# Kernel tuning notes

Hardware: AMD Instinct MI355X
Metric: run time of the kernel (lower is better)

## Reference

```python
import jax, jax.numpy as jnp
import numpy as np

HIDDEN = 1024
NUM_HEADS = 16
HEAD_SIZE = HIDDEN // NUM_HEADS
B, S = 2, 2048


def setup_inputs() -> dict:
    key = jax.random.key(0)
    k_x, k_wqkv, k_bqkv, k_wo, k_bo = jax.random.split(key, 5)
    x = jax.random.normal(k_x, (B, S, HIDDEN), dtype=jnp.float32)
    # Dense kernels, fan-in scaled like lecun_normal init
    Wqkv = jax.random.normal(k_wqkv, (HIDDEN, 3 * HIDDEN), dtype=jnp.float32) / np.sqrt(HIDDEN)
    bqkv = jnp.zeros((3 * HIDDEN,), dtype=jnp.float32)
    Wo = jax.random.normal(k_wo, (HIDDEN, HIDDEN), dtype=jnp.float32) / np.sqrt(HIDDEN)
    bo = jnp.zeros((HIDDEN,), dtype=jnp.float32)
    return {"x": x, "Wqkv": Wqkv, "bqkv": bqkv, "Wo": Wo, "bo": bo}


def reference(x, Wqkv, bqkv, Wo, bo):
    b, s, h = x.shape
    qkv = jnp.einsum('bsh,hf->bsf', x, Wqkv) + bqkv          # [b, s, 3*h]
    qkv = qkv.reshape(b, s, 3, NUM_HEADS, HEAD_SIZE)
    q, k, v = qkv[:, :, 0], qkv[:, :, 1], qkv[:, :, 2]        # [b, s, nh, hd]
    scale = 1.0 / np.sqrt(HEAD_SIZE)
    scores = jnp.einsum('bqhd,bkhd->bhqk', q, k) * scale      # [b, nh, s, s]
    weights = jax.nn.softmax(scores, axis=-1)
    attn = jnp.einsum('bhqk,bkhd->bqhd', weights, v)          # [b, s, nh, hd]
    attn = attn.reshape(b, s, h)
    return jnp.einsum('bsh,hf->bsf', attn, Wo) + bo
```

## Files before the change

### kernel.cpp

```cpp
#include <hip/hip_runtime.h>
#include <hip/hip_bf16.h>

#define HIDDEN 1024
#define NH 16
#define BATCH 2
#define SEQ 2048

typedef __attribute__((ext_vector_type(8))) short bf16x8;
typedef __attribute__((ext_vector_type(4))) float f32x4;

__device__ __forceinline__ ushort f2bf(float f) {
    __hip_bfloat16 h = __float2bfloat16(f);
    return *reinterpret_cast<ushort*>(&h);
}
__device__ __forceinline__ float fexp2(float x) {
#if __has_builtin(__builtin_amdgcn_exp2f)
    return __builtin_amdgcn_exp2f(x);
#else
    return exp2f(x);
#endif
}
__device__ __forceinline__ uint pack_bf_trunc(float a, float b) {
    return __builtin_amdgcn_perm(__float_as_uint(b), __float_as_uint(a), 0x07060302u);
}

__device__ __forceinline__ void async_copy16(const ushort* g, ushort* l) {
    __builtin_amdgcn_global_load_lds((const __attribute__((address_space(1))) void*)g,
                                     (__attribute__((address_space(3))) void*)l,
                                     16, 0, 0);
}

__global__ void prep_kernel(const float* __restrict__ x,
                            const float* __restrict__ Wqkv,
                            const float* __restrict__ Wo,
                            ushort* __restrict__ xb,
                            ushort* __restrict__ Wt,
                            ushort* __restrict__ WoT)
{
    __shared__ float t[32][33];
    const int bid = blockIdx.x;
    const int tid = threadIdx.x;

    if (bid < 4096) {
        int i = (bid * 256 + tid) * 4;
        float4 v = *(const float4*)(x + i);
        ushort4 w;
        w.x = f2bf(v.x); w.y = f2bf(v.y); w.z = f2bf(v.z); w.w = f2bf(v.w);
        *(ushort4*)(xb + i) = w;
        return;
    }
    const int r = tid >> 3;
    const int c = (tid & 7) * 4;
    if (bid < 7168) {
        int tt = bid - 4096;
        int k0 = (tt & 31) * 32;
        int n0 = (tt >> 5) * 32;
        const int N = 3 * HIDDEN, K = HIDDEN;
        float4 v = *(const float4*)(Wqkv + (size_t)(k0 + r) * N + n0 + c);
        t[r][c] = v.x; t[r][c + 1] = v.y; t[r][c + 2] = v.z; t[r][c + 3] = v.w;
        __syncthreads();
        ushort4 w;
        w.x = f2bf(t[c + 0][r]); w.y = f2bf(t[c + 1][r]);
        w.z = f2bf(t[c + 2][r]); w.w = f2bf(t[c + 3][r]);
        *(ushort4*)(Wt + (size_t)(n0 + r) * K + k0 + c) = w;
    } else {
        int tt = bid - 7168;
        int k0 = (tt & 31) * 32;
        int n0 = (tt >> 5) * 32;
        const int N = HIDDEN, K = HIDDEN;
        float4 v = *(const float4*)(Wo + (size_t)(k0 + r) * N + n0 + c);
        t[r][c] = v.x; t[r][c + 1] = v.y; t[r][c + 2] = v.z; t[r][c + 3] = v.w;
        __syncthreads();
        ushort4 w;
        w.x = f2bf(t[c + 0][r]); w.y = f2bf(t[c + 1][r]);
        w.z = f2bf(t[c + 2][r]); w.w = f2bf(t[c + 3][r]);
        *(ushort4*)(WoT + (size_t)(n0 + r) * K + k0 + c) = w;
    }
}

__global__ __launch_bounds__(256, 3)
void gemm_mfma_bf16_kernel(const ushort* __restrict__ A,
                           const ushort* __restrict__ Bt,
                           const float* __restrict__ bias,
                           ushort* __restrict__ C, int N,
                           int qscale_cols, float qscale,
                           ushort* __restrict__ vtg, int vt_mode)
{
    constexpr int K = 1024;
    __shared__ ushort As[128 * 64];
    __shared__ ushort Bs[128 * 64];

    const int tid  = threadIdx.x;
    const int wave = tid >> 6;
    const int lane = tid & 63;
    const int l16  = lane & 15;
    const int quad = lane >> 4;
    const int wm = wave & 1, wn = wave >> 1;

    const int bm = blockIdx.y * 128;
    const int bn = blockIdx.x * 128;

    const int srow = lane >> 3;
    const int lblk = (lane & 7) ^ srow;
    const ushort* Ag = A  + (size_t)(bm + wave * 32 + srow) * K + lblk * 8;
    const ushort* Bg = Bt + (size_t)(bn + wave * 32 + srow) * K + lblk * 8;
    ushort* Asl = As + wave * 32 * 64;
    ushort* Bsl = Bs + wave * 32 * 64;

    f32x4 acc[4][4];
    #pragma unroll
    for (int i = 0; i < 4; i++)
        #pragma unroll
        for (int j = 0; j < 4; j++) acc[i][j] = (f32x4){0.f, 0.f, 0.f, 0.f};

    for (int k0 = 0; k0 < K; k0 += 64) {
        __syncthreads();
        #pragma unroll
        for (int t = 0; t < 4; t++) {
            async_copy16(Ag + (size_t)t * 8 * K + k0, Asl + t * 8 * 64);
            async_copy16(Bg + (size_t)t * 8 * K + k0, Bsl + t * 8 * 64);
        }
        __syncthreads();

        #pragma unroll
        for (int s = 0; s < 2; s++) {
            bf16x8 af[4], bfr[4];
            #pragma unroll
            for (int i = 0; i < 4; i++) {
                int m = wm * 64 + i * 16 + l16;
                int n = wn * 64 + i * 16 + l16;
                af[i]  = *(const bf16x8*)&As[m * 64 + (((s * 4 + quad) ^ (m & 7)) << 3)];
                bfr[i] = *(const bf16x8*)&Bs[n * 64 + (((s * 4 + quad) ^ (n & 7)) << 3)];
            }
            #pragma unroll
            for (int i = 0; i < 4; i++)
                #pragma unroll
                for (int j = 0; j < 4; j++)
                    acc[i][j] = __builtin_amdgcn_mfma_f32_16x16x32_bf16(af[i], bfr[j], acc[i][j], 0, 0, 0);
        }
    }

    #pragma unroll
    for (int j = 0; j < 4; j++) {
        int col = bn + wn * 64 + j * 16 + l16;
        float bv = bias[col];
        if (vt_mode && col >= 2048) {
            int dfull = col - 2048;
            int hh = dfull >> 6, dd = dfull & 63;
            int bb = bm >> 11;
            int sb = ((bm & 2047) + wm * 64) >> 6;
            ushort tmp[16];
            #pragma unroll
            for (int i = 0; i < 4; i++)
                #pragma unroll
                for (int r = 0; r < 4; r++)
                    tmp[r * 4 + i] = f2bf(acc[i][j][r] + bv);
            ushort* dst = vtg + ((size_t)((bb * NH + hh) * 64 + dd)) * SEQ
                          + sb * 64 + quad * 16;
            *(uint4*)dst = *(const uint4*)tmp;
            *(uint4*)(dst + 8) = *(const uint4*)(tmp + 8);
        } else {
            float s = (col < qscale_cols) ? qscale : 1.0f;
            #pragma unroll
            for (int i = 0; i < 4; i++) {
                int row0 = bm + wm * 64 + i * 16 + quad * 4;
                #pragma unroll
                for (int r = 0; r < 4; r++)
                    C[(size_t)(row0 + r) * N + col] = f2bf((acc[i][j][r] + bv) * s);
            }
        }
    }
}

__global__ __launch_bounds__(256, 4)
void gemm_out_kernel(const ushort* __restrict__ A,
                     const ushort* __restrict__ Bt,
                     const float* __restrict__ bias,
                     float* __restrict__ C)
{
    constexpr int K = 1024, N = 1024;
    __shared__ ushort As[128 * 64];
    __shared__ ushort Bs[64 * 64];

    const int tid  = threadIdx.x;
    const int wave = tid >> 6;
    const int lane = tid & 63;
    const int l16  = lane & 15;
    const int quad = lane >> 4;
    const int wm = wave & 1, wn = wave >> 1;

    const int bm = blockIdx.y * 128;
    const int bn = blockIdx.x * 64;

    const int srow = lane >> 3;
    const int lblk = (lane & 7) ^ srow;
    const ushort* Ag = A  + (size_t)(bm + wave * 32 + srow) * K + lblk * 8;
    const ushort* Bg = Bt + (size_t)(bn + wave * 16 + srow) * K + lblk * 8;
    ushort* Asl = As + wave * 32 * 64;
    ushort* Bsl = Bs + wave * 16 * 64;

    f32x4 acc[4][2];
    #pragma unroll
    for (int i = 0; i < 4; i++)
        #pragma unroll
        for (int j = 0; j < 2; j++) acc[i][j] = (f32x4){0.f, 0.f, 0.f, 0.f};

    for (int k0 = 0; k0 < K; k0 += 64) {
        __syncthreads();
        #pragma unroll
        for (int t = 0; t < 4; t++)
            async_copy16(Ag + (size_t)t * 8 * K + k0, Asl + t * 8 * 64);
        #pragma unroll
        for (int t = 0; t < 2; t++)
            async_copy16(Bg + (size_t)t * 8 * K + k0, Bsl + t * 8 * 64);
        __syncthreads();

        #pragma unroll
        for (int s = 0; s < 2; s++) {
            bf16x8 af[4], bfr[2];
            #pragma unroll
            for (int i = 0; i < 4; i++) {
                int m = wm * 64 + i * 16 + l16;
                af[i] = *(const bf16x8*)&As[m * 64 + (((s * 4 + quad) ^ (m & 7)) << 3)];
            }
            #pragma unroll
            for (int j = 0; j < 2; j++) {
                int n = wn * 32 + j * 16 + l16;
                bfr[j] = *(const bf16x8*)&Bs[n * 64 + (((s * 4 + quad) ^ (n & 7)) << 3)];
            }
            #pragma unroll
            for (int i = 0; i < 4; i++)
                #pragma unroll
                for (int j = 0; j < 2; j++)
                    acc[i][j] = __builtin_amdgcn_mfma_f32_16x16x32_bf16(af[i], bfr[j], acc[i][j], 0, 0, 0);
        }
    }

    #pragma unroll
    for (int j = 0; j < 2; j++) {
        int col = bn + wn * 32 + j * 16 + l16;
        float bv = bias[col];
        #pragma unroll
        for (int i = 0; i < 4; i++) {
            int row0 = bm + wm * 64 + i * 16 + quad * 4;
            #pragma unroll
            for (int r = 0; r < 4; r++)
                C[(size_t)(row0 + r) * N + col] = acc[i][j][r] + bv;
        }
    }
}

__global__ __launch_bounds__(256, 2)
void attn_mfma_v8_kernel(const ushort* __restrict__ qkvb,
                         const ushort* __restrict__ vtg,
                         ushort* __restrict__ attn)
{
    __shared__ __align__(16) ushort smem[34816];

    const int tid  = threadIdx.x;
    const int wave = tid >> 6;
    const int qg   = wave & 1;
    const int kh   = wave >> 1;
    const int lane = tid & 63;
    const int l16  = lane & 15;
    const int quad = lane >> 4;

    const int obid = blockIdx.x;
    const int qb = (obid >> 3) & 15;
    const int bh = (obid & 7) * 4 + (obid >> 7);
    const int h  = bh & (NH - 1);
    const int b  = bh >> 4;

    const int qbase = qb * 128 + qg * 64;
    const int hoff  = h * 64;

    ushort* KsH = smem + kh * 4096;
    ushort* VsH = smem + 8192 + kh * 4096;
    ushort* Psw = smem + 16384 + wave * 4608;

    bf16x8 a_q[4][2];
    #pragma unroll
    for (int mg = 0; mg < 4; mg++) {
        int qrow = b * SEQ + qbase + mg * 16 + l16;
        const ushort* qp = qkvb + (size_t)qrow * 3072 + hoff + quad * 8;
        a_q[mg][0] = *(const bf16x8*)qp;
        a_q[mg][1] = *(const bf16x8*)(qp + 32);
    }

    f32x4 o[4][4];
    f32x4 lacc[4];
    #pragma unroll
    for (int mg = 0; mg < 4; mg++) {
        lacc[mg] = (f32x4){0.f, 0.f, 0.f, 0.f};
        #pragma unroll
        for (int nt = 0; nt < 4; nt++) o[mg][nt] = (f32x4){0.f, 0.f, 0.f, 0.f};
    }

    bf16x8 b_ones;
    #pragma unroll
    for (int j = 0; j < 8; j++) b_ones[j] = (short)0x3f80;

    const ushort* kvb    = qkvb + (size_t)b * SEQ * 3072;
    const ushort* vtg_bh = vtg + (size_t)((b * NH + h) * 64) * SEQ;

    const int srow8 = lane >> 3;
    const int gblk  = ((lane & 7) ^ srow8) << 3;
    const ushort* kg = kvb + (size_t)(kh * 1024 + qg * 32 + srow8) * 3072 + 1024 + hoff + gblk;
    const ushort* vg = vtg_bh + (size_t)(qg * 32 + srow8) * SEQ + kh * 1024 + gblk;

    for (int t = 0; t < 16; t++) {
        const int k0 = t * 64;
        __syncthreads();
        #pragma unroll
        for (int c = 0; c < 4; c++) {
            async_copy16(kg + (size_t)(k0 + c * 8) * 3072, KsH + (qg * 32 + c * 8) * 64);
            async_copy16(vg + (size_t)(c * 8) * SEQ + k0,  VsH + (qg * 32 + c * 8) * 64);
        }
        __syncthreads();

        f32x4 sc[4][4];
        #pragma unroll
        for (int nt = 0; nt < 4; nt++) {
            int key = nt * 16 + l16;
            bf16x8 bk0 = *(const bf16x8*)&KsH[key * 64 + ((quad ^ (key & 7)) << 3)];
            bf16x8 bk1 = *(const bf16x8*)&KsH[key * 64 + (((4 + quad) ^ (key & 7)) << 3)];
            #pragma unroll
            for (int mg = 0; mg < 4; mg++) {
                f32x4 a = (f32x4){0.f, 0.f, 0.f, 0.f};
                a = __builtin_amdgcn_mfma_f32_16x16x32_bf16(a_q[mg][0], bk0, a, 0, 0, 0);
                a = __builtin_amdgcn_mfma_f32_16x16x32_bf16(a_q[mg][1], bk1, a, 0, 0, 0);
                sc[mg][nt] = a;
            }
        }

        #pragma unroll
        for (int mg = 0; mg < 4; mg++) {
            #pragma unroll
            for (int r = 0; r < 4; r++) {
                int q = mg * 16 + quad * 4 + r;
                uint2 pk2;
                pk2.x = pack_bf_trunc(fexp2(sc[mg][0][r]), fexp2(sc[mg][1][r]));
                pk2.y = pack_bf_trunc(fexp2(sc[mg][2][r]), fexp2(sc[mg][3][r]));
                *(uint2*)&Psw[q * 72 + l16 * 4] = pk2;
            }
        }

        asm volatile("s_waitcnt lgkmcnt(0)" ::: "memory");

        #pragma unroll
        for (int mg = 0; mg < 4; mg++) {
            bf16x8 ap0 = *(const bf16x8*)&Psw[(mg * 16 + l16) * 72 + quad * 8];
            bf16x8 ap1 = *(const bf16x8*)&Psw[(mg * 16 + l16) * 72 + 32 + quad * 8];
            #pragma unroll
            for (int nt = 0; nt < 4; nt++) {
                int d = nt * 16 + l16;
                bf16x8 bv0 = *(const bf16x8*)&VsH[d * 64 + ((quad ^ (d & 7)) << 3)];
                bf16x8 bv1 = *(const bf16x8*)&VsH[d * 64 + (((4 + quad) ^ (d & 7)) << 3)];
                o[mg][nt] = __builtin_amdgcn_mfma_f32_16x16x32_bf16(ap0, bv0, o[mg][nt], 0, 0, 0);
                o[mg][nt] = __builtin_amdgcn_mfma_f32_16x16x32_bf16(ap1, bv1, o[mg][nt], 0, 0, 0);
            }
            lacc[mg] = __builtin_amdgcn_mfma_f32_16x16x32_bf16(ap0, b_ones, lacc[mg], 0, 0, 0);
            lacc[mg] = __builtin_amdgcn_mfma_f32_16x16x32_bf16(ap1, b_ones, lacc[mg], 0, 0, 0);
        }
    }

    __syncthreads();
    float* osc = (float*)smem;
    float* lsc = (float*)(smem + 16384);
    const int ob = qg * 4096;
    const int lb = qg * 64;
    if (kh == 1) {
        #pragma unroll
        for (int mg = 0; mg < 4; mg++) {
            #pragma unroll
            for (int nt = 0; nt < 4; nt++)
                *(f32x4*)&osc[ob + ((mg * 4 + nt) * 4 + quad) * 64 + l16 * 4] = o[mg][nt];
            if (l16 == 0) *(f32x4*)&lsc[lb + (mg * 4 + quad) * 4] = lacc[mg];
        }
    }
    __syncthreads();
    if (kh == 0) {
        #pragma unroll
        for (int mg = 0; mg < 4; mg++) {
            #pragma unroll
            for (int nt = 0; nt < 4; nt++)
                o[mg][nt] += *(const f32x4*)&osc[ob + ((mg * 4 + nt) * 4 + quad) * 64 + l16 * 4];
            lacc[mg] += *(const f32x4*)&lsc[lb + (mg * 4 + quad) * 4];
        }
        #pragma unroll
        for (int mg = 0; mg < 4; mg++) {
            #pragma unroll
            for (int r = 0; r < 4; r++) {
                float inv = 1.f / lacc[mg][r];
                int row = b * SEQ + qbase + mg * 16 + quad * 4 + r;
                size_t base = (size_t)row * HIDDEN + hoff + l16;
                #pragma unroll
                for (int nt = 0; nt < 4; nt++)
                    attn[base + nt * 16] = f2bf(o[mg][nt][r] * inv);
            }
        }
    }
}

__global__ __launch_bounds__(512, 4)
void attn_mfma_fb_kernel(const ushort* __restrict__ qkvb,
                         ushort* __restrict__ attn)
{
    __shared__ __align__(16) ushort smem[34816];

    const int tid   = threadIdx.x;
    const int wave  = tid >> 6;
    const int wavel = wave & 3;
    const int kh    = wave >> 2;
    const int lane  = tid & 63;
    const int l16   = lane & 15;
    const int quad  = lane >> 4;

    const int qb = blockIdx.x & 15;
    const int bh = blockIdx.x >> 4;
    const int h  = bh & (NH - 1);
    const int b  = bh >> 4;

    const int qbase = qb * 128;
    const int hoff  = h * 64;

    ushort* KsH = smem + kh * 4096;
    ushort* VsH = smem + 8192 + kh * 4096;
    ushort* Psw = smem + 16384 + wave * 2304;

    bf16x8 a_q[2][2];
    #pragma unroll
    for (int mg = 0; mg < 2; mg++) {
        int qrow = b * SEQ + qbase + wavel * 32 + mg * 16 + l16;
        const ushort* qp = qkvb + (size_t)qrow * 3072 + hoff + quad * 8;
        a_q[mg][0] = *(const bf16x8*)qp;
        a_q[mg][1] = *(const bf16x8*)(qp + 32);
    }

    f32x4 o[2][4];
    f32x4 lacc[2];
    #pragma unroll
    for (int mg = 0; mg < 2; mg++) {
        lacc[mg] = (f32x4){0.f, 0.f, 0.f, 0.f};
        #pragma unroll
        for (int nt = 0; nt < 4; nt++) o[mg][nt] = (f32x4){0.f, 0.f, 0.f, 0.f};
    }

    bf16x8 b_ones;
    #pragma unroll
    for (int j = 0; j < 8; j++) b_ones[j] = (short)0x3f80;

    const ushort* kvb = qkvb + (size_t)b * SEQ * 3072;

    for (int t = 0; t < 16; t++) {
        const int k0 = t * 64;
        __syncthreads();
        {
            const int tl = tid & 255;
            #pragma unroll
            for (int i = 0; i < 2; i++) {
                int key = (tl >> 3) + 32 * i;
                int blk = tl & 7;
                const ushort* ksrc = kvb + (size_t)(kh * 1024 + k0 + key) * 3072 + 1024 + hoff + blk * 8;
                uint4 kv = *(const uint4*)ksrc;
                *(uint4*)&KsH[key * 64 + ((blk ^ (key & 7)) << 3)] = kv;
                uint4 vv = *(const uint4*)(ksrc + 1024);
                const ushort* vpp = (const ushort*)&vv;
                int pk_ = (key & 15) * 4 + (key >> 4);
                #pragma unroll
                for (int j = 0; j < 8; j++) {
                    int d = blk * 8 + j;
                    VsH[d * 64 + (((pk_ >> 3) ^ (d & 7)) << 3) + (pk_ & 7)] = vpp[j];
                }
            }
        }
        __syncthreads();

        f32x4 sc[2][4];
        #pragma unroll
        for (int nt = 0; nt < 4; nt++) {
            int key = nt * 16 + l16;
            bf16x8 bk0 = *(const bf16x8*)&KsH[key * 64 + ((quad ^ (key & 7)) << 3)];
            bf16x8 bk1 = *(const bf16x8*)&KsH[key * 64 + (((4 + quad) ^ (key & 7)) << 3)];
            #pragma unroll
            for (int mg = 0; mg < 2; mg++) {
                f32x4 a = (f32x4){0.f, 0.f, 0.f, 0.f};
                a = __builtin_amdgcn_mfma_f32_16x16x32_bf16(a_q[mg][0], bk0, a, 0, 0, 0);
                a = __builtin_amdgcn_mfma_f32_16x16x32_bf16(a_q[mg][1], bk1, a, 0, 0, 0);
                sc[mg][nt] = a;
            }
        }

        #pragma unroll
        for (int mg = 0; mg < 2; mg++) {
            #pragma unroll
            for (int r = 0; r < 4; r++) {
                int q = mg * 16 + quad * 4 + r;
                uint2 pk2;
                pk2.x = pack_bf_trunc(fexp2(sc[mg][0][r]), fexp2(sc[mg][1][r]));
                pk2.y = pack_bf_trunc(fexp2(sc[mg][2][r]), fexp2(sc[mg][3][r]));
                *(uint2*)&Psw[q * 72 + l16 * 4] = pk2;
            }
        }

        asm volatile("s_waitcnt lgkmcnt(0)" ::: "memory");
        bf16x8 a_p[2][2];
        #pragma unroll
        for (int mg = 0; mg < 2; mg++) {
            a_p[mg][0] = *(const bf16x8*)&Psw[(mg * 16 + l16) * 72 + quad * 8];
            a_p[mg][1] = *(const bf16x8*)&Psw[(mg * 16 + l16) * 72 + 32 + quad * 8];
        }

        #pragma unroll
        for (int nt = 0; nt < 4; nt++) {
            int d = nt * 16 + l16;
            bf16x8 bv0 = *(const bf16x8*)&VsH[d * 64 + ((quad ^ (d & 7)) << 3)];
            bf16x8 bv1 = *(const bf16x8*)&VsH[d * 64 + (((4 + quad) ^ (d & 7)) << 3)];
            #pragma unroll
            for (int mg = 0; mg < 2; mg++) {
                o[mg][nt] = __builtin_amdgcn_mfma_f32_16x16x32_bf16(a_p[mg][0], bv0, o[mg][nt], 0, 0, 0);
                o[mg][nt] = __builtin_amdgcn_mfma_f32_16x16x32_bf16(a_p[mg][1], bv1, o[mg][nt], 0, 0, 0);
            }
        }
        #pragma unroll
        for (int mg = 0; mg < 2; mg++) {
            lacc[mg] = __builtin_amdgcn_mfma_f32_16x16x32_bf16(a_p[mg][0], b_ones, lacc[mg], 0, 0, 0);
            lacc[mg] = __builtin_amdgcn_mfma_f32_16x16x32_bf16(a_p[mg][1], b_ones, lacc[mg], 0, 0, 0);
        }
    }

    __syncthreads();
    float* osc = (float*)smem;
    float* lsc = (float*)(smem + 16384);
    const int fo = wavel * 2048 + quad * 64 + l16 * 4;
    const int fl = wavel * 512 + quad * 64 + l16 * 4;
    if (kh == 1) {
        #pragma unroll
        for (int mg = 0; mg < 2; mg++) {
            #pragma unroll
            for (int nt = 0; nt < 4; nt++)
                *(f32x4*)&osc[fo + (mg * 4 + nt) * 256] = o[mg][nt];
            *(f32x4*)&lsc[fl + mg * 256] = lacc[mg];
        }
    }
    __syncthreads();
    if (kh == 0) {
        #pragma unroll
        for (int mg = 0; mg < 2; mg++) {
            #pragma unroll
            for (int nt = 0; nt < 4; nt++)
                o[mg][nt] += *(const f32x4*)&osc[fo + (mg * 4 + nt) * 256];
            lacc[mg] += *(const f32x4*)&lsc[fl + mg * 256];
        }
        #pragma unroll
        for (int mg = 0; mg < 2; mg++) {
            #pragma unroll
            for (int r = 0; r < 4; r++) {
                float inv = 1.f / lacc[mg][r];
                int row = b * SEQ + qbase + wavel * 32 + mg * 16 + quad * 4 + r;
                size_t base = (size_t)row * HIDDEN + hoff + l16;
                #pragma unroll
                for (int nt = 0; nt < 4; nt++)
                    attn[base + nt * 16] = f2bf(o[mg][nt][r] * inv);
            }
        }
    }
}

extern "C" void kernel_launch(void* const* d_in, const int* in_sizes, int n_in,
                              void* d_out, int out_size, void* d_ws, size_t ws_size,
                              hipStream_t stream) {
    const float* x    = (const float*)d_in[0];
    const float* Wqkv = (const float*)d_in[1];
    const float* bqkv = (const float*)d_in[2];
    const float* Wo   = (const float*)d_in[3];
    const float* bo   = (const float*)d_in[4];
    float* out = (float*)d_out;

    const int M = BATCH * SEQ;
    const size_t MB = 1024 * 1024;

    char* ws = (char*)d_ws;
    ushort* qkvb = (ushort*)ws;
    ushort* attn = (ushort*)(ws + 24 * MB);
    ushort* xb   = (ushort*)(ws + 24 * MB);
    ushort* Wt   = (ushort*)(ws + 32 * MB);
    ushort* WoT  = (ushort*)(ws + 38 * MB);
    ushort* vtg  = (ushort*)(ws + 40 * MB);
    const int use_vtg = (ws_size >= 48 * MB) ? 1 : 0;

    const float qscale = 0.125f * 1.44269504088896f;

    prep_kernel<<<8192, 256, 0, stream>>>(x, Wqkv, Wo, xb, Wt, WoT);

    {
        dim3 grid((3 * HIDDEN) / 128, M / 128);
        gemm_mfma_bf16_kernel<<<grid, 256, 0, stream>>>(xb, Wt, bqkv, qkvb,
                                                        3 * HIDDEN, HIDDEN, qscale,
                                                        vtg, use_vtg);
    }

    if (use_vtg) {
        attn_mfma_v8_kernel<<<BATCH * NH * (SEQ / 128), 256, 0, stream>>>(
            qkvb, vtg, attn);
    } else {
        attn_mfma_fb_kernel<<<BATCH * NH * (SEQ / 128), 512, 0, stream>>>(
            qkvb, attn);
    }

    {
        dim3 grid(HIDDEN / 64, M / 128);
        gemm_out_kernel<<<grid, 256, 0, stream>>>(attn, WoT, bo, out);
    }
}
```

Before: 181.0 us.

## Restructure attention to 8 waves with 16 queries each and double-buffered K/V

Replaces the 4-wave attention kernel, in which each wave held 64 queries and the key range was split across wave pairs, with an 8-wave kernel where each wave owns 16 queries and all waves share a full-key-range loop. K/V tiles are double-buffered in shared memory, so the next tile's async copy is issued before the current tile is computed, and the cross-wave O/l reduction at the end is removed. Registers per wave and LDS per block shrink, allowing more waves resident. In exchange each wave reuses every K/V LDS read across only 16 queries instead of 64, which raises LDS read traffic per MFMA.

```diff
diff --git a/kernel.cpp b/kernel.cpp
--- a/kernel.cpp
+++ b/kernel.cpp
@@ -250,17 +250,15 @@
     }
 }
 
-__global__ __launch_bounds__(256, 2)
-void attn_mfma_v8_kernel(const ushort* __restrict__ qkvb,
+__global__ __launch_bounds__(512, 4)
+void attn_mfma_v9_kernel(const ushort* __restrict__ qkvb,
                          const ushort* __restrict__ vtg,
                          ushort* __restrict__ attn)
 {
-    __shared__ __align__(16) ushort smem[34816];
+    __shared__ __align__(16) ushort smem[25600];
 
     const int tid  = threadIdx.x;
     const int wave = tid >> 6;
-    const int qg   = wave & 1;
-    const int kh   = wave >> 1;
     const int lane = tid & 63;
     const int l16  = lane & 15;
     const int quad = lane >> 4;
@@ -271,30 +269,23 @@
     const int h  = bh & (NH - 1);
     const int b  = bh >> 4;
 
-    const int qbase = qb * 128 + qg * 64;
+    const int qbase = qb * 128 + wave * 16;
     const int hoff  = h * 64;
 
-    ushort* KsH = smem + kh * 4096;
-    ushort* VsH = smem + 8192 + kh * 4096;
-    ushort* Psw = smem + 16384 + wave * 4608;
-
-    bf16x8 a_q[4][2];
-    #pragma unroll
-    for (int mg = 0; mg < 4; mg++) {
-        int qrow = b * SEQ + qbase + mg * 16 + l16;
+    ushort* Psw = smem + 16384 + wave * 1152;
+
+    bf16x8 a_q0, a_q1;
+    {
+        int qrow = b * SEQ + qbase + l16;
         const ushort* qp = qkvb + (size_t)qrow * 3072 + hoff + quad * 8;
-        a_q[mg][0] = *(const bf16x8*)qp;
-        a_q[mg][1] = *(const bf16x8*)(qp + 32);
-    }
-
-    f32x4 o[4][4];
-    f32x4 lacc[4];
-    #pragma unroll
-    for (int mg = 0; mg < 4; mg++) {
-        lacc[mg] = (f32x4){0.f, 0.f, 0.f, 0.f};
-        #pragma unroll
-        for (int nt = 0; nt < 4; nt++) o[mg][nt] = (f32x4){0.f, 0.f, 0.f, 0.f};
-    }
+        a_q0 = *(const bf16x8*)qp;
+        a_q1 = *(const bf16x8*)(qp + 32);
+    }
+
+    f32x4 o[4];
+    f32x4 lacc = (f32x4){0.f, 0.f, 0.f, 0.f};
+    #pragma unroll
+    for (int nt = 0; nt < 4; nt++) o[nt] = (f32x4){0.f, 0.f, 0.f, 0.f};
 
     bf16x8 b_ones;
     #pragma unroll
@@ -305,100 +296,74 @@
 
     const int srow8 = lane >> 3;
     const int gblk  = ((lane & 7) ^ srow8) << 3;
-    const ushort* kg = kvb + (size_t)(kh * 1024 + qg * 32 + srow8) * 3072 + 1024 + hoff + gblk;
-    const ushort* vg = vtg_bh + (size_t)(qg * 32 + srow8) * SEQ + kh * 1024 + gblk;
-
-    for (int t = 0; t < 16; t++) {
-        const int k0 = t * 64;
-        __syncthreads();
-        #pragma unroll
-        for (int c = 0; c < 4; c++) {
-            async_copy16(kg + (size_t)(k0 + c * 8) * 3072, KsH + (qg * 32 + c * 8) * 64);
-            async_copy16(vg + (size_t)(c * 8) * SEQ + k0,  VsH + (qg * 32 + c * 8) * 64);
-        }
-        __syncthreads();
-
-        f32x4 sc[4][4];
+    const ushort* kg = kvb + (size_t)(wave * 8 + srow8) * 3072 + 1024 + hoff + gblk;
+    const ushort* vg = vtg_bh + (size_t)(wave * 8 + srow8) * SEQ + gblk;
+
+    ushort* k_dst = smem + wave * 512;
+    ushort* v_dst = smem + 8192 + wave * 512;
+
+    async_copy16(kg, k_dst);
+    async_copy16(vg, v_dst);
+    __syncthreads();
+
+    int cur = 0;
+    for (int t = 0; t < 32; t++) {
+        if (t < 31) {
+            const int k0n = (t + 1) * 64;
+            async_copy16(kg + (size_t)k0n * 3072, k_dst + ((cur ^ 1) << 12));
+            async_copy16(vg + k0n,                v_dst + ((cur ^ 1) << 12));
+        }
+        const ushort* Ks = smem + (cur << 12);
+        const ushort* Vs = smem + 8192 + (cur << 12);
+
+        f32x4 sc[4];
         #pragma unroll
         for (int nt = 0; nt < 4; nt++) {
             int key = nt * 16 + l16;
-            bf16x8 bk0 = *(const bf16x8*)&KsH[key * 64 + ((quad ^ (key & 7)) << 3)];
-            bf16x8 bk1 = *(const bf16x8*)&KsH[key * 64 + (((4 + quad) ^ (key & 7)) << 3)];
-            #pragma unroll
-            for (int mg = 0; mg < 4; mg++) {
-                f32x4 a = (f32x4){0.f, 0.f, 0.f, 0.f};
-                a = __builtin_amdgcn_mfma_f32_16x16x32_bf16(a_q[mg][0], bk0, a, 0, 0, 0);
-                a = __builtin_amdgcn_mfma_f32_16x16x32_bf16(a_q[mg][1], bk1, a, 0, 0, 0);
-                sc[mg][nt] = a;
-            }
-        }
-
-        #pragma unroll
-        for (int mg = 0; mg < 4; mg++) {
-            #pragma unroll
-            for (int r = 0; r < 4; r++) {
-                int q = mg * 16 + quad * 4 + r;
-                uint2 pk2;
-                pk2.x = pack_bf_trunc(fexp2(sc[mg][0][r]), fexp2(sc[mg][1][r]));
-                pk2.y = pack_bf_trunc(fexp2(sc[mg][2][r]), fexp2(sc[mg][3][r]));
-                *(uint2*)&Psw[q * 72 + l16 * 4] = pk2;
-            }
+            bf16x8 bk0 = *(const bf16x8*)&Ks[key * 64 + ((quad ^ (key & 7)) << 3)];
+            bf16x8 bk1 = *(const bf16x8*)&Ks[key * 64 + (((4 + quad) ^ (key & 7)) << 3)];
+            f32x4 a = (f32x4){0.f, 0.f, 0.f, 0.f};
+            a = __builtin_amdgcn_mfma_f32_16x16x32_bf16(a_q0, bk0, a, 0, 0, 0);
+            a = __builtin_amdgcn_mfma_f32_16x16x32_bf16(a_q1, bk1, a, 0, 0, 0);
+            sc[nt] = a;
+        }
+
+        #pragma unroll
+        for (int r = 0; r < 4; r++) {
+            int q = quad * 4 + r;
+            uint2 pk2;
+            pk2.x = pack_bf_trunc(fexp2(sc[0][r]), fexp2(sc[1][r]));
+            pk2.y = pack_bf_trunc(fexp2(sc[2][r]), fexp2(sc[3][r]));
+            *(uint2*)&Psw[q * 72 + l16 * 4] = pk2;
         }
 
         asm volatile("s_waitcnt lgkmcnt(0)" ::: "memory");
 
-        #pragma unroll
-        for (int mg = 0; mg < 4; mg++) {
-            bf16x8 ap0 = *(const bf16x8*)&Psw[(mg * 16 + l16) * 72 + quad * 8];
-            bf16x8 ap1 = *(const bf16x8*)&Psw[(mg * 16 + l16) * 72 + 32 + quad * 8];
-            #pragma unroll
-            for (int nt = 0; nt < 4; nt++) {
-                int d = nt * 16 + l16;
-                bf16x8 bv0 = *(const bf16x8*)&VsH[d * 64 + ((quad ^ (d & 7)) << 3)];
-                bf16x8 bv1 = *(const bf16x8*)&VsH[d * 64 + (((4 + quad) ^ (d & 7)) << 3)];
-                o[mg][nt] = __builtin_amdgcn_mfma_f32_16x16x32_bf16(ap0, bv0, o[mg][nt], 0, 0, 0);
-                o[mg][nt] = __builtin_amdgcn_mfma_f32_16x16x32_bf16(ap1, bv1, o[mg][nt], 0, 0, 0);
-            }
-            lacc[mg] = __builtin_amdgcn_mfma_f32_16x16x32_bf16(ap0, b_ones, lacc[mg], 0, 0, 0);
-            lacc[mg] = __builtin_amdgcn_mfma_f32_16x16x32_bf16(ap1, b_ones, lacc[mg], 0, 0, 0);
-        }
-    }
-
-    __syncthreads();
-    float* osc = (float*)smem;
-    float* lsc = (float*)(smem + 16384);
-    const int ob = qg * 4096;
-    const int lb = qg * 64;
-    if (kh == 1) {
-        #pragma unroll
-        for (int mg = 0; mg < 4; mg++) {
-            #pragma unroll
-            for (int nt = 0; nt < 4; nt++)
-                *(f32x4*)&osc[ob + ((mg * 4 + nt) * 4 + quad) * 64 + l16 * 4] = o[mg][nt];
-            if (l16 == 0) *(f32x4*)&lsc[lb + (mg * 4 + quad) * 4] = lacc[mg];
-        }
-    }
-    __syncthreads();
-    if (kh == 0) {
-        #pragma unroll
-        for (int mg = 0; mg < 4; mg++) {
-            #pragma unroll
-            for (int nt = 0; nt < 4; nt++)
-                o[mg][nt] += *(const f32x4*)&osc[ob + ((mg * 4 + nt) * 4 + quad) * 64 + l16 * 4];
-            lacc[mg] += *(const f32x4*)&lsc[lb + (mg * 4 + quad) * 4];
-        }
-        #pragma unroll
-        for (int mg = 0; mg < 4; mg++) {
-            #pragma unroll
-            for (int r = 0; r < 4; r++) {
-                float inv = 1.f / lacc[mg][r];
-                int row = b * SEQ + qbase + mg * 16 + quad * 4 + r;
-                size_t base = (size_t)row * HIDDEN + hoff + l16;
-                #pragma unroll
-                for (int nt = 0; nt < 4; nt++)
-                    attn[base + nt * 16] = f2bf(o[mg][nt][r] * inv);
-            }
-        }
+        bf16x8 ap0 = *(const bf16x8*)&Psw[l16 * 72 + quad * 8];
+        bf16x8 ap1 = *(const bf16x8*)&Psw[l16 * 72 + 32 + quad * 8];
+        #pragma unroll
+        for (int nt = 0; nt < 4; nt++) {
+            int d = nt * 16 + l16;
+            bf16x8 bv0 = *(const bf16x8*)&Vs[d * 64 + ((quad ^ (d & 7)) << 3)];
+            bf16x8 bv1 = *(const bf16x8*)&Vs[d * 64 + (((4 + quad) ^ (d & 7)) << 3)];
+            o[nt] = __builtin_amdgcn_mfma_f32_16x16x32_bf16(ap0, bv0, o[nt], 0, 0, 0);
+            o[nt] = __builtin_amdgcn_mfma_f32_16x16x32_bf16(ap1, bv1, o[nt], 0, 0, 0);
+        }
+        lacc = __builtin_amdgcn_mfma_f32_16x16x32_bf16(ap0, b_ones, lacc, 0, 0, 0);
+        lacc = __builtin_amdgcn_mfma_f32_16x16x32_bf16(ap1, b_ones, lacc, 0, 0, 0);
+
+        __syncthreads();
+        cur ^= 1;
+    }
+
+    #pragma unroll
+    for (int r = 0; r < 4; r++) {
+        float inv = 1.f / lacc[r];
+        int row = b * SEQ + qbase + quad * 4 + r;
+        size_t base = (size_t)row * HIDDEN + hoff + l16;
+        #pragma unroll
+        for (int nt = 0; nt < 4; nt++)
+            attn[base + nt * 16] = f2bf(o[nt][r] * inv);
     }
 }
 
@@ -601,7 +566,7 @@
     }
 
     if (use_vtg) {
-        attn_mfma_v8_kernel<<<BATCH * NH * (SEQ / 128), 256, 0, stream>>>(
+        attn_mfma_v9_kernel<<<BATCH * NH * (SEQ / 128), 512, 0, stream>>>(
             qkvb, vtg, attn);
     } else {
         attn_mfma_fb_kernel<<<BATCH * NH * (SEQ / 128), 512, 0, stream>>>(
```

Result: no change. 178.3 us (-1.5%).

## Restructure attention kernel: per-wave query split with double-buffered K/V tiles

Applied to the files above, without the earlier changes.

The attention kernel no longer splits the key range across two wave halves, which had to be merged through shared memory at the end. Each of the four waves now owns 32 query rows and walks all 2048 keys. K/V tiles are shared by all waves and double-buffered, so the next tile's async copy is issued while the current one is computed, leaving one barrier per iteration instead of two. This drops the cross-wave reduction and overlaps loads with math, at the cost of fewer rows per wave, which reduces reuse of each K/V fragment loaded from LDS.

```diff
diff --git a/kernel.cpp b/kernel.cpp
--- a/kernel.cpp
+++ b/kernel.cpp
@@ -251,16 +251,14 @@
 }
 
 __global__ __launch_bounds__(256, 2)
-void attn_mfma_v8_kernel(const ushort* __restrict__ qkvb,
-                         const ushort* __restrict__ vtg,
-                         ushort* __restrict__ attn)
+void attn_mfma_v10_kernel(const ushort* __restrict__ qkvb,
+                          const ushort* __restrict__ vtg,
+                          ushort* __restrict__ attn)
 {
-    __shared__ __align__(16) ushort smem[34816];
+    __shared__ __align__(16) ushort smem[25600];
 
     const int tid  = threadIdx.x;
     const int wave = tid >> 6;
-    const int qg   = wave & 1;
-    const int kh   = wave >> 1;
     const int lane = tid & 63;
     const int l16  = lane & 15;
     const int quad = lane >> 4;
@@ -271,26 +269,24 @@
     const int h  = bh & (NH - 1);
     const int b  = bh >> 4;
 
-    const int qbase = qb * 128 + qg * 64;
+    const int qbase = qb * 128 + wave * 32;
     const int hoff  = h * 64;
 
-    ushort* KsH = smem + kh * 4096;
-    ushort* VsH = smem + 8192 + kh * 4096;
-    ushort* Psw = smem + 16384 + wave * 4608;
-
-    bf16x8 a_q[4][2];
-    #pragma unroll
-    for (int mg = 0; mg < 4; mg++) {
+    ushort* Psw = smem + 16384 + wave * 2304;
+
+    bf16x8 a_q[2][2];
+    #pragma unroll
+    for (int mg = 0; mg < 2; mg++) {
         int qrow = b * SEQ + qbase + mg * 16 + l16;
         const ushort* qp = qkvb + (size_t)qrow * 3072 + hoff + quad * 8;
         a_q[mg][0] = *(const bf16x8*)qp;
         a_q[mg][1] = *(const bf16x8*)(qp + 32);
     }
 
-    f32x4 o[4][4];
-    f32x4 lacc[4];
-    #pragma unroll
-    for (int mg = 0; mg < 4; mg++) {
+    f32x4 o[2][4];
+    f32x4 lacc[2];
+    #pragma unroll
+    for (int mg = 0; mg < 2; mg++) {
         lacc[mg] = (f32x4){0.f, 0.f, 0.f, 0.f};
         #pragma unroll
         for (int nt = 0; nt < 4; nt++) o[mg][nt] = (f32x4){0.f, 0.f, 0.f, 0.f};
@@ -305,27 +301,42 @@
 
     const int srow8 = lane >> 3;
     const int gblk  = ((lane & 7) ^ srow8) << 3;
-    const ushort* kg = kvb + (size_t)(kh * 1024 + qg * 32 + srow8) * 3072 + 1024 + hoff + gblk;
-    const ushort* vg = vtg_bh + (size_t)(qg * 32 + srow8) * SEQ + kh * 1024 + gblk;
-
-    for (int t = 0; t < 16; t++) {
-        const int k0 = t * 64;
-        __syncthreads();
-        #pragma unroll
-        for (int c = 0; c < 4; c++) {
-            async_copy16(kg + (size_t)(k0 + c * 8) * 3072, KsH + (qg * 32 + c * 8) * 64);
-            async_copy16(vg + (size_t)(c * 8) * SEQ + k0,  VsH + (qg * 32 + c * 8) * 64);
-        }
-        __syncthreads();
-
-        f32x4 sc[4][4];
+    const ushort* kg = kvb + (size_t)(wave * 16 + srow8) * 3072 + 1024 + hoff + gblk;
+    const ushort* vg = vtg_bh + (size_t)(wave * 16 + srow8) * SEQ + gblk;
+
+    ushort* k_dst = smem + wave * 1024;
+    ushort* v_dst = smem + 8192 + wave * 1024;
+
+    #pragma unroll
+    for (int c = 0; c < 2; c++) {
+        async_copy16(kg + (size_t)(c * 8) * 3072, k_dst + c * 512);
+        async_copy16(vg + (size_t)(c * 8) * SEQ,  v_dst + c * 512);
+    }
+    __syncthreads();
+
+    int cur = 0;
+    for (int t = 0; t < 32; t++) {
+        if (t < 31) {
+            const int k0n = (t + 1) * 64;
+            #pragma unroll
+            for (int c = 0; c < 2; c++) {
+                async_copy16(kg + (size_t)(k0n + c * 8) * 3072,
+                             k_dst + c * 512 + ((cur ^ 1) << 12));
+                async_copy16(vg + (size_t)(c * 8) * SEQ + k0n,
+                             v_dst + c * 512 + ((cur ^ 1) << 12));
+            }
+        }
+        const ushort* Ks = smem + (cur << 12);
+        const ushort* Vs = smem + 8192 + (cur << 12);
+
+        f32x4 sc[2][4];
         #pragma unroll
         for (int nt = 0; nt < 4; nt++) {
             int key = nt * 16 + l16;
-            bf16x8 bk0 = *(const bf16x8*)&KsH[key * 64 + ((quad ^ (key & 7)) << 3)];
-            bf16x8 bk1 = *(const bf16x8*)&KsH[key * 64 + (((4 + quad) ^ (key & 7)) << 3)];
-            #pragma unroll
-            for (int mg = 0; mg < 4; mg++) {
+            bf16x8 bk0 = *(const bf16x8*)&Ks[key * 64 + ((quad ^ (key & 7)) << 3)];
+            bf16x8 bk1 = *(const bf16x8*)&Ks[key * 64 + (((4 + quad) ^ (key & 7)) << 3)];
+            #pragma unroll
+            for (int mg = 0; mg < 2; mg++) {
                 f32x4 a = (f32x4){0.f, 0.f, 0.f, 0.f};
                 a = __builtin_amdgcn_mfma_f32_16x16x32_bf16(a_q[mg][0], bk0, a, 0, 0, 0);
                 a = __builtin_amdgcn_mfma_f32_16x16x32_bf16(a_q[mg][1], bk1, a, 0, 0, 0);
@@ -334,7 +345,7 @@
         }
 
         #pragma unroll
-        for (int mg = 0; mg < 4; mg++) {
+        for (int mg = 0; mg < 2; mg++) {
             #pragma unroll
             for (int r = 0; r < 4; r++) {
                 int q = mg * 16 + quad * 4 + r;
@@ -347,57 +358,43 @@
 
         asm volatile("s_waitcnt lgkmcnt(0)" ::: "memory");
 
-        #pragma unroll
-        for (int mg = 0; mg < 4; mg++) {
-            bf16x8 ap0 = *(const bf16x8*)&Psw[(mg * 16 + l16) * 72 + quad * 8];
-            bf16x8 ap1 = *(const bf16x8*)&Psw[(mg * 16 + l16) * 72 + 32 + quad * 8];
-            #pragma unroll
-            for (int nt = 0; nt < 4; nt++) {
-                int d = nt * 16 + l16;
-                bf16x8 bv0 = *(const bf16x8*)&VsH[d * 64 + ((quad ^ (d & 7)) << 3)];
-                bf16x8 bv1 = *(const bf16x8*)&VsH[d * 64 + (((4 + quad) ^ (d & 7)) << 3)];
-                o[mg][nt] = __builtin_amdgcn_mfma_f32_16x16x32_bf16(ap0, bv0, o[mg][nt], 0, 0, 0);
-                o[mg][nt] = __builtin_amdgcn_mfma_f32_16x16x32_bf16(ap1, bv1, o[mg][nt], 0, 0, 0);
-            }
-            lacc[mg] = __builtin_amdgcn_mfma_f32_16x16x32_bf16(ap0, b_ones, lacc[mg], 0, 0, 0);
-            lacc[mg] = __builtin_amdgcn_mfma_f32_16x16x32_bf16(ap1, b_ones, lacc[mg], 0, 0, 0);
-        }
-    }
-
-    __syncthreads();
-    float* osc = (float*)smem;
-    float* lsc = (float*)(smem + 16384);
-    const int ob = qg * 4096;
-    const int lb = qg * 64;
-    if (kh == 1) {
-        #pragma unroll
-        for (int mg = 0; mg < 4; mg++) {
+        bf16x8 ap[2][2];
+        #pragma unroll
+        for (int mg = 0; mg < 2; mg++) {
+            ap[mg][0] = *(const bf16x8*)&Psw[(mg * 16 + l16) * 72 + quad * 8];
+            ap[mg][1] = *(const bf16x8*)&Psw[(mg * 16 + l16) * 72 + 32 + quad * 8];
+        }
+        #pragma unroll
+        for (int nt = 0; nt < 4; nt++) {
+            int d = nt * 16 + l16;
+            bf16x8 bv0 = *(const bf16x8*)&Vs[d * 64 + ((quad ^ (d & 7)) << 3)];
+            bf16x8 bv1 = *(const bf16x8*)&Vs[d * 64 + (((4 + quad) ^ (d & 7)) << 3)];
+            #pragma unroll
+            for (int mg = 0; mg < 2; mg++) {
+                o[mg][nt] = __builtin_amdgcn_mfma_f32_16x16x32_bf16(ap[mg][0], bv0, o[mg][nt], 0, 0, 0);
+                o[mg][nt] = __builtin_amdgcn_mfma_f32_16x16x32_bf16(ap[mg][1], bv1, o[mg][nt], 0, 0, 0);
+            }
+        }
+        #pragma unroll
+        for (int mg = 0; mg < 2; mg++) {
+            lacc[mg] = __builtin_amdgcn_mfma_f32_16x16x32_bf16(ap[mg][0], b_ones, lacc[mg], 0, 0, 0);
+            lacc[mg] = __builtin_amdgcn_mfma_f32_16x16x32_bf16(ap[mg][1], b_ones, lacc[mg], 0, 0, 0);
+        }
+
+        __syncthreads();
+        cur ^= 1;
+    }
+
+    #pragma unroll
+    for (int mg = 0; mg < 2; mg++) {
+        #pragma unroll
+        for (int r = 0; r < 4; r++) {
+            float inv = 1.f / lacc[mg][r];
+            int row = b * SEQ + qbase + mg * 16 + quad * 4 + r;
+            size_t base = (size_t)row * HIDDEN + hoff + l16;
             #pragma unroll
             for (int nt = 0; nt < 4; nt++)
-                *(f32x4*)&osc[ob + ((mg * 4 + nt) * 4 + quad) * 64 + l16 * 4] = o[mg][nt];
-            if (l16 == 0) *(f32x4*)&lsc[lb + (mg * 4 + quad) * 4] = lacc[mg];
-        }
-    }
-    __syncthreads();
-    if (kh == 0) {
-        #pragma unroll
-        for (int mg = 0; mg < 4; mg++) {
-            #pragma unroll
-            for (int nt = 0; nt < 4; nt++)
-                o[mg][nt] += *(const f32x4*)&osc[ob + ((mg * 4 + nt) * 4 + quad) * 64 + l16 * 4];
-            lacc[mg] += *(const f32x4*)&lsc[lb + (mg * 4 + quad) * 4];
-        }
-        #pragma unroll
-        for (int mg = 0; mg < 4; mg++) {
-            #pragma unroll
-            for (int r = 0; r < 4; r++) {
-                float inv = 1.f / lacc[mg][r];
-                int row = b * SEQ + qbase + mg * 16 + quad * 4 + r;
-                size_t base = (size_t)row * HIDDEN + hoff + l16;
-                #pragma unroll
-                for (int nt = 0; nt < 4; nt++)
-                    attn[base + nt * 16] = f2bf(o[mg][nt][r] * inv);
-            }
+                attn[base + nt * 16] = f2bf(o[mg][nt][r] * inv);
         }
     }
 }
@@ -601,7 +598,7 @@
     }
 
     if (use_vtg) {
-        attn_mfma_v8_kernel<<<BATCH * NH * (SEQ / 128), 256, 0, stream>>>(
+        attn_mfma_v10_kernel<<<BATCH * NH * (SEQ / 128), 256, 0, stream>>>(
             qkvb, vtg, attn);
     } else {
         attn_mfma_fb_kernel<<<BATCH * NH * (SEQ / 128), 512, 0, stream>>>(
```

After: 177.1 us. 2.2% less time.
